# Performance work log

Hardware: AMD Instinct MI355X
Metric: run time of the kernel (lower is better)

Reference implementation:

```python
import jax, jax.numpy as jnp
import numpy as np

B = 512
IN_F = 512
OUT_F = 512
NOISE = 128
OUT_DIM = IN_F * OUT_F + OUT_F  # 262656
PRIOR_SCALE = 1.0


def setup_inputs() -> dict:
    key = jax.random.key(0)
    k_x, k_px, k_n, k_w, k_b, k_pw = jax.random.split(key, 6)
    x = jax.random.normal(k_x, (B, IN_F), dtype=jnp.float32)
    prior_x = jax.random.normal(k_px, (B, IN_F), dtype=jnp.float32)
    hyper_noise = jax.random.normal(k_n, (B, NOISE), dtype=jnp.float32)
    # nn.Linear default init: U(-1/sqrt(fan_in), 1/sqrt(fan_in))
    lim = 1.0 / np.sqrt(NOISE)
    hyper_W = jax.random.uniform(k_w, (OUT_DIM, NOISE), dtype=jnp.float32, minval=-lim, maxval=lim)
    hyper_b = jax.random.uniform(k_b, (OUT_DIM,), dtype=jnp.float32, minval=-lim, maxval=lim)
    # PriorHyperLinear: row-normalized gaussian weight (prior_std=1 -> identity scale), zero bias
    pw = jax.random.normal(k_pw, (OUT_DIM, NOISE), dtype=jnp.float32)
    prior_W = pw / jnp.linalg.norm(pw, axis=1, keepdims=True)
    prior_b = jnp.zeros((OUT_DIM,), dtype=jnp.float32)
    return {"x": x, "prior_x": prior_x, "hyper_noise": hyper_noise,
            "hyper_W": hyper_W, "hyper_b": hyper_b,
            "prior_W": prior_W, "prior_b": prior_b}


def _base_forward(x, params):
    # params: [B, IN_F*OUT_F + OUT_F]
    w = params[:, : IN_F * OUT_F].reshape(-1, IN_F, OUT_F)  # [B, in, out]
    b = params[:, IN_F * OUT_F:]                            # [B, out]
    # bmm([B,1,in],[B,in,out]) + bias -> squeeze -> [B, out]
    return jnp.einsum('bi,bio->bo', x, w) + b


def reference(x, prior_x, hyper_noise, hyper_W, hyper_b, prior_W, prior_b):
    params = hyper_noise @ hyper_W.T + hyper_b            # [B, OUT_DIM]
    out = _base_forward(x, params)
    prior_params = hyper_noise @ prior_W.T + prior_b      # [B, OUT_DIM]
    out = out + _base_forward(prior_x, prior_params) * PRIOR_SCALE
    return out
```

## Files before the change

### kernel.cpp

```cpp
#include <hip/hip_runtime.h>
#include <hip/hip_fp16.h>


#define MAIN_D (512*512)

typedef _Float16 half8 __attribute__((ext_vector_type(8)));
typedef float floatx4 __attribute__((ext_vector_type(4)));

static __device__ __forceinline__ unsigned pk2(float a, float b) {
    union { __half2 h; unsigned u; } c;
    c.h = __float22half2_rn(make_float2(a, b));
    return c.u;
}

__global__ __launch_bounds__(256) void init_kernel(
    const float* __restrict__ hb, const float* __restrict__ pb,
    float* __restrict__ out)
{
    const int idx = blockIdx.x * 256 + threadIdx.x;
    const int o4 = (idx * 4) & 511;
    float4 v;
    v.x = hb[MAIN_D + o4 + 0] + pb[MAIN_D + o4 + 0];
    v.y = hb[MAIN_D + o4 + 1] + pb[MAIN_D + o4 + 1];
    v.z = hb[MAIN_D + o4 + 2] + pb[MAIN_D + o4 + 2];
    v.w = hb[MAIN_D + o4 + 3] + pb[MAIN_D + o4 + 3];
    *(float4*)(out + idx * 4) = v;
}

__global__ __launch_bounds__(512, 2) void main_gemm(
    const float* __restrict__ x, const float* __restrict__ px,
    const float* __restrict__ noise,
    const float* __restrict__ hW, const float* __restrict__ hb,
    const float* __restrict__ pW, const float* __restrict__ pb,
    float* __restrict__ out)
{
    __shared__ __attribute__((aligned(16))) _Float16 Bl[2][128 * 136];
    __shared__ __attribute__((aligned(16))) _Float16 xhl[256 * 40];

    const int t = threadIdx.x;
    const int lin  = blockIdx.x;
    const int s    = (lin >> 3) & 1;
    const int g    = ((lin >> 4) << 3) | (lin & 7);
    const int z    = g >> 2;
    const int y    = g & 3;
    const int b0   = s * 256;
    const int o0   = y * 128;
    const int branch = z >> 4;
    const int ic0  = (z & 15) * 32;
    const float* __restrict__ xsrc = branch ? px : x;
    const float* __restrict__ Ws   = branch ? pW : hW;
    const float* __restrict__ bias = branch ? pb : hb;
    const int nmacro = ((z & 15) == 0) ? 33 : 32;

#pragma unroll
    for (int k = 0; k < 4; ++k) {
        int idx = k * 512 + t;
        int bb = idx >> 3, c = (idx & 7) * 4;
        float4 v = *(const float4*)(xsrc + (b0 + bb) * 512 + ic0 + c);
        *(unsigned*)&xhl[bb * 40 + c]     = pk2(v.x, v.y);
        *(unsigned*)&xhl[bb * 40 + c + 2] = pk2(v.z, v.w);
    }
    _Float16* nzl = &Bl[0][0];
#pragma unroll
    for (int k = 0; k < 16; ++k) {
        int idx = k * 512 + t;
        int bb = idx >> 5, c = (idx & 31) * 4;
        float4 v = *(const float4*)(noise + (b0 + bb) * 128 + c);
        *(unsigned*)&nzl[bb * 136 + c]     = pk2(v.x, v.y);
        *(unsigned*)&nzl[bb * 136 + c + 2] = pk2(v.z, v.w);
    }
    __syncthreads();

    const int lane = t & 63;
    const int w    = t >> 6;
    const int wm64 = (w >> 1) * 64;
    const int wn64 = (w & 1) * 64;
    const int quad = lane >> 4;
    const int l16  = lane & 15;

    half8 nzf[4][4];
#pragma unroll
    for (int mf = 0; mf < 4; ++mf)
#pragma unroll
        for (int q = 0; q < 4; ++q)
            nzf[mf][q] = *(half8*)&nzl[(wm64 + mf * 16 + l16) * 136 + q * 32 + quad * 8];

    floatx4 acc[4][4];
#pragma unroll
    for (int a = 0; a < 4; ++a)
#pragma unroll
        for (int b = 0; b < 4; ++b) acc[a][b] = (floatx4)0.0f;

    float4 wa[4], wb[4];
    {
        const float* p = Ws + (long)(ic0 * 512 + o0) * 128;
#pragma unroll
        for (int j = 0; j < 4; ++j) {
            int c = j * 512 + t;
            int off = (c >> 4) * 128 + (c & 15) * 8;
            wa[j] = *(const float4*)(p + off);
            wb[j] = *(const float4*)(p + off + 4);
        }
    }
    __syncthreads();

    for (int m = 0; m < nmacro; ++m) {
        _Float16* buf = &Bl[m & 1][0];
#pragma unroll
        for (int j = 0; j < 4; ++j) {
            int c = j * 512 + t;
            int row = c >> 4, col8 = (c & 15) * 8;
            *(uint4*)&buf[row * 136 + col8] = make_uint4(
                pk2(wa[j].x, wa[j].y), pk2(wa[j].z, wa[j].w),
                pk2(wb[j].x, wb[j].y), pk2(wb[j].z, wb[j].w));
        }
        __syncthreads();
        if (m + 1 < nmacro) {
            long rb = (m + 1 < 32) ? (long)((ic0 + m + 1) * 512 + o0)
                                   : (long)(MAIN_D + o0);
            const float* p = Ws + rb * 128;
#pragma unroll
            for (int j = 0; j < 4; ++j) {
                int c = j * 512 + t;
                int off = (c >> 4) * 128 + (c & 15) * 8;
                wa[j] = *(const float4*)(p + off);
                wb[j] = *(const float4*)(p + off + 4);
            }
        }
        const bool isE2 = (m >= 32);
        _Float16 xs[4];
        if (!isE2) {
#pragma unroll
            for (int mf = 0; mf < 4; ++mf)
                xs[mf] = xhl[(wm64 + mf * 16 + l16) * 40 + m];
        }
#pragma unroll
        for (int q = 0; q < 4; ++q) {
            half8 bfr[4], afr[4];
#pragma unroll
            for (int nf = 0; nf < 4; ++nf)
                bfr[nf] = *(half8*)&buf[(wn64 + nf * 16 + l16) * 136 + q * 32 + quad * 8];
#pragma unroll
            for (int mf = 0; mf < 4; ++mf) {
                if (isE2) afr[mf] = nzf[mf][q];
                else {
                    half8 xv;
#pragma unroll
                    for (int j = 0; j < 8; ++j) xv[j] = xs[mf];
                    afr[mf] = nzf[mf][q] * xv;
                }
            }
#pragma unroll
            for (int mf = 0; mf < 4; ++mf)
#pragma unroll
                for (int nf = 0; nf < 4; ++nf)
                    acc[mf][nf] = __builtin_amdgcn_mfma_f32_16x16x32_f16(
                        afr[mf], bfr[nf], acc[mf][nf], 0, 0, 0);
        }
    }

    __syncthreads();
    {
        const int oo = t >> 2, kh = (t & 3) * 8;
        float tmp[8];
#pragma unroll
        for (int j = 0; j < 8; ++j)
            tmp[j] = bias[(long)(ic0 + kh + j) * 512 + o0 + oo];
        *(uint4*)&Bl[0][oo * 136 + kh] = make_uint4(
            pk2(tmp[0], tmp[1]), pk2(tmp[2], tmp[3]),
            pk2(tmp[4], tmp[5]), pk2(tmp[6], tmp[7]));
    }
    __syncthreads();
    {
        half8 afr[4], bfr[4];
#pragma unroll
        for (int mf = 0; mf < 4; ++mf)
            afr[mf] = *(half8*)&xhl[(wm64 + mf * 16 + l16) * 40 + quad * 8];
#pragma unroll
        for (int nf = 0; nf < 4; ++nf)
            bfr[nf] = *(half8*)&Bl[0][(wn64 + nf * 16 + l16) * 136 + quad * 8];
#pragma unroll
        for (int mf = 0; mf < 4; ++mf)
#pragma unroll
            for (int nf = 0; nf < 4; ++nf)
                acc[mf][nf] = __builtin_amdgcn_mfma_f32_16x16x32_f16(
                    afr[mf], bfr[nf], acc[mf][nf], 0, 0, 0);
    }

#pragma unroll
    for (int mf = 0; mf < 4; ++mf)
#pragma unroll
        for (int nf = 0; nf < 4; ++nf)
#pragma unroll
            for (int r = 0; r < 4; ++r) {
                int row = b0 + wm64 + mf * 16 + quad * 4 + r;
                int col = o0 + wn64 + nf * 16 + l16;
                atomicAdd(out + row * 512 + col, acc[mf][nf][r]);
            }
}

extern "C" void kernel_launch(void* const* d_in, const int* in_sizes, int n_in,
                              void* d_out, int out_size, void* d_ws, size_t ws_size,
                              hipStream_t stream) {
    const float* x  = (const float*)d_in[0];
    const float* px = (const float*)d_in[1];
    const float* nz = (const float*)d_in[2];
    const float* hW = (const float*)d_in[3];
    const float* hb = (const float*)d_in[4];
    const float* pW = (const float*)d_in[5];
    const float* pb = (const float*)d_in[6];
    float* out = (float*)d_out;

    hipLaunchKernelGGL(init_kernel, dim3(256), dim3(256), 0, stream, hb, pb, out);
    hipLaunchKernelGGL(main_gemm, dim3(256), dim3(512), 0, stream,
                       x, px, nz, hW, hb, pW, pb, out);
}
```

Baseline: 319.9 us.

## Halve output tile width to double grid size and raise occupancy

Shrinks each block's output tile from 128 to 64 columns, doubling the grid to 512 blocks and raising launch bounds to 4 blocks per CU with smaller LDS buffers. Noise fragments are now loaded straight from global memory into registers instead of staging through shared memory, which removes one barrier. MFMA sections are wrapped in s_setprio to favour the matrix issue. The aim is to fill all CUs and hide the memory-bound weight stream. The cost is that noise and x are re-read by twice as many blocks, and there are twice as many atomic adds to the output.

New measurement: 421.5 us. +31.8%, slower.

```diff
diff --git a/kernel.cpp b/kernel.cpp
--- a/kernel.cpp
+++ b/kernel.cpp
@@ -11,6 +11,12 @@
     union { __half2 h; unsigned u; } c;
     c.h = __float22half2_rn(make_float2(a, b));
     return c.u;
+}
+
+static __device__ __forceinline__ half8 mk8(float4 a, float4 b) {
+    union { uint4 u; half8 h; } r;
+    r.u = make_uint4(pk2(a.x, a.y), pk2(a.z, a.w), pk2(b.x, b.y), pk2(b.z, b.w));
+    return r.h;
 }
 
 __global__ __launch_bounds__(256) void init_kernel(
@@ -27,24 +33,24 @@
     *(float4*)(out + idx * 4) = v;
 }
 
-__global__ __launch_bounds__(512, 2) void main_gemm(
+__global__ __launch_bounds__(512, 4) void main_gemm(
     const float* __restrict__ x, const float* __restrict__ px,
     const float* __restrict__ noise,
     const float* __restrict__ hW, const float* __restrict__ hb,
     const float* __restrict__ pW, const float* __restrict__ pb,
     float* __restrict__ out)
 {
-    __shared__ __attribute__((aligned(16))) _Float16 Bl[2][128 * 136];
+    __shared__ __attribute__((aligned(16))) _Float16 Bl[2][64 * 136];
     __shared__ __attribute__((aligned(16))) _Float16 xhl[256 * 40];
 
     const int t = threadIdx.x;
     const int lin  = blockIdx.x;
     const int s    = (lin >> 3) & 1;
     const int g    = ((lin >> 4) << 3) | (lin & 7);
-    const int z    = g >> 2;
-    const int y    = g & 3;
+    const int y    = g & 7;
+    const int z    = g >> 3;
     const int b0   = s * 256;
-    const int o0   = y * 128;
+    const int o0   = y * 64;
     const int branch = z >> 4;
     const int ic0  = (z & 15) * 32;
     const float* __restrict__ xsrc = branch ? px : x;
@@ -52,6 +58,13 @@
     const float* __restrict__ bias = branch ? pb : hb;
     const int nmacro = ((z & 15) == 0) ? 33 : 32;
 
+    const int lane = t & 63;
+    const int w    = t >> 6;
+    const int wm64 = (w >> 1) * 64;
+    const int wn32 = (w & 1) * 32;
+    const int quad = lane >> 4;
+    const int l16  = lane & 15;
+
 #pragma unroll
     for (int k = 0; k < 4; ++k) {
         int idx = k * 512 + t;
@@ -60,54 +73,39 @@
         *(unsigned*)&xhl[bb * 40 + c]     = pk2(v.x, v.y);
         *(unsigned*)&xhl[bb * 40 + c + 2] = pk2(v.z, v.w);
     }
-    _Float16* nzl = &Bl[0][0];
-#pragma unroll
-    for (int k = 0; k < 16; ++k) {
-        int idx = k * 512 + t;
-        int bb = idx >> 5, c = (idx & 31) * 4;
-        float4 v = *(const float4*)(noise + (b0 + bb) * 128 + c);
-        *(unsigned*)&nzl[bb * 136 + c]     = pk2(v.x, v.y);
-        *(unsigned*)&nzl[bb * 136 + c + 2] = pk2(v.z, v.w);
-    }
-    __syncthreads();
-
-    const int lane = t & 63;
-    const int w    = t >> 6;
-    const int wm64 = (w >> 1) * 64;
-    const int wn64 = (w & 1) * 64;
-    const int quad = lane >> 4;
-    const int l16  = lane & 15;
 
     half8 nzf[4][4];
 #pragma unroll
     for (int mf = 0; mf < 4; ++mf)
 #pragma unroll
-        for (int q = 0; q < 4; ++q)
-            nzf[mf][q] = *(half8*)&nzl[(wm64 + mf * 16 + l16) * 136 + q * 32 + quad * 8];
-
-    floatx4 acc[4][4];
+        for (int q = 0; q < 4; ++q) {
+            const float* np = noise + (long)(b0 + wm64 + mf * 16 + l16) * 128
+                            + q * 32 + quad * 8;
+            nzf[mf][q] = mk8(*(const float4*)np, *(const float4*)(np + 4));
+        }
+
+    floatx4 acc[4][2];
 #pragma unroll
     for (int a = 0; a < 4; ++a)
 #pragma unroll
-        for (int b = 0; b < 4; ++b) acc[a][b] = (floatx4)0.0f;
-
-    float4 wa[4], wb[4];
+        for (int b = 0; b < 2; ++b) acc[a][b] = (floatx4)0.0f;
+
+    float4 wa[2], wb[2];
     {
         const float* p = Ws + (long)(ic0 * 512 + o0) * 128;
 #pragma unroll
-        for (int j = 0; j < 4; ++j) {
+        for (int j = 0; j < 2; ++j) {
             int c = j * 512 + t;
             int off = (c >> 4) * 128 + (c & 15) * 8;
             wa[j] = *(const float4*)(p + off);
             wb[j] = *(const float4*)(p + off + 4);
         }
     }
-    __syncthreads();
 
     for (int m = 0; m < nmacro; ++m) {
         _Float16* buf = &Bl[m & 1][0];
 #pragma unroll
-        for (int j = 0; j < 4; ++j) {
+        for (int j = 0; j < 2; ++j) {
             int c = j * 512 + t;
             int row = c >> 4, col8 = (c & 15) * 8;
             *(uint4*)&buf[row * 136 + col8] = make_uint4(
@@ -120,7 +118,7 @@
                                    : (long)(MAIN_D + o0);
             const float* p = Ws + rb * 128;
 #pragma unroll
-            for (int j = 0; j < 4; ++j) {
+            for (int j = 0; j < 2; ++j) {
                 int c = j * 512 + t;
                 int off = (c >> 4) * 128 + (c & 15) * 8;
                 wa[j] = *(const float4*)(p + off);
@@ -136,10 +134,10 @@
         }
 #pragma unroll
         for (int q = 0; q < 4; ++q) {
-            half8 bfr[4], afr[4];
-#pragma unroll
-            for (int nf = 0; nf < 4; ++nf)
-                bfr[nf] = *(half8*)&buf[(wn64 + nf * 16 + l16) * 136 + q * 32 + quad * 8];
+            half8 bfr[2], afr[4];
+#pragma unroll
+            for (int nf = 0; nf < 2; ++nf)
+                bfr[nf] = *(half8*)&buf[(wn32 + nf * 16 + l16) * 136 + q * 32 + quad * 8];
 #pragma unroll
             for (int mf = 0; mf < 4; ++mf) {
                 if (isE2) afr[mf] = nzf[mf][q];
@@ -150,39 +148,40 @@
                     afr[mf] = nzf[mf][q] * xv;
                 }
             }
+            __builtin_amdgcn_s_setprio(1);
 #pragma unroll
             for (int mf = 0; mf < 4; ++mf)
 #pragma unroll
-                for (int nf = 0; nf < 4; ++nf)
+                for (int nf = 0; nf < 2; ++nf)
                     acc[mf][nf] = __builtin_amdgcn_mfma_f32_16x16x32_f16(
                         afr[mf], bfr[nf], acc[mf][nf], 0, 0, 0);
+            __builtin_amdgcn_s_setprio(0);
         }
     }
 
     __syncthreads();
     {
-        const int oo = t >> 2, kh = (t & 3) * 8;
-        float tmp[8];
-#pragma unroll
-        for (int j = 0; j < 8; ++j)
+        const int oo = t >> 3, kh = (t & 7) * 4;
+        float tmp[4];
+#pragma unroll
+        for (int j = 0; j < 4; ++j)
             tmp[j] = bias[(long)(ic0 + kh + j) * 512 + o0 + oo];
-        *(uint4*)&Bl[0][oo * 136 + kh] = make_uint4(
-            pk2(tmp[0], tmp[1]), pk2(tmp[2], tmp[3]),
-            pk2(tmp[4], tmp[5]), pk2(tmp[6], tmp[7]));
+        *(uint2*)&Bl[0][oo * 136 + kh] = make_uint2(
+            pk2(tmp[0], tmp[1]), pk2(tmp[2], tmp[3]));
     }
     __syncthreads();
     {
-        half8 afr[4], bfr[4];
+        half8 afr[4], bfr[2];
 #pragma unroll
         for (int mf = 0; mf < 4; ++mf)
             afr[mf] = *(half8*)&xhl[(wm64 + mf * 16 + l16) * 40 + quad * 8];
 #pragma unroll
-        for (int nf = 0; nf < 4; ++nf)
-            bfr[nf] = *(half8*)&Bl[0][(wn64 + nf * 16 + l16) * 136 + quad * 8];
+        for (int nf = 0; nf < 2; ++nf)
+            bfr[nf] = *(half8*)&Bl[0][(wn32 + nf * 16 + l16) * 136 + quad * 8];
 #pragma unroll
         for (int mf = 0; mf < 4; ++mf)
 #pragma unroll
-            for (int nf = 0; nf < 4; ++nf)
+            for (int nf = 0; nf < 2; ++nf)
                 acc[mf][nf] = __builtin_amdgcn_mfma_f32_16x16x32_f16(
                     afr[mf], bfr[nf], acc[mf][nf], 0, 0, 0);
     }
@@ -190,11 +189,11 @@
 #pragma unroll
     for (int mf = 0; mf < 4; ++mf)
 #pragma unroll
-        for (int nf = 0; nf < 4; ++nf)
+        for (int nf = 0; nf < 2; ++nf)
 #pragma unroll
             for (int r = 0; r < 4; ++r) {
                 int row = b0 + wm64 + mf * 16 + quad * 4 + r;
-                int col = o0 + wn64 + nf * 16 + l16;
+                int col = o0 + wn32 + nf * 16 + l16;
                 atomicAdd(out + row * 512 + col, acc[mf][nf][r]);
             }
 }
@@ -212,6 +211,6 @@
     float* out = (float*)d_out;
 
     hipLaunchKernelGGL(init_kernel, dim3(256), dim3(256), 0, stream, hb, pb, out);
-    hipLaunchKernelGGL(main_gemm, dim3(256), dim3(512), 0, stream,
+    hipLaunchKernelGGL(main_gemm, dim3(512), dim3(512), 0, stream,
                        x, px, nz, hW, hb, pW, pb, out);
 }
```

## Split batch into 128-row tiles, doubling grid, load noise directly to registers

Applied to the files above, without the earlier changes.

The batch tile per block is halved from 256 to 128 rows, and the grid doubles to 512 blocks, so each wave holds a 32x64 accumulator tile instead of 64x64. The noise fragments are now loaded straight from global memory into registers rather than staged through LDS, which removes one barrier. The MFMA sections are wrapped in s_setprio, and launch bounds request 4 blocks per CU. The aim is more occupancy and parallelism, but every weight tile is now streamed by twice as many blocks, which doubles global weight traffic and the number of atomic adds.

Measured after the change: 342.9 us. 1.07x slower.

```diff
diff --git a/kernel.cpp b/kernel.cpp
--- a/kernel.cpp
+++ b/kernel.cpp
@@ -11,6 +11,12 @@
     union { __half2 h; unsigned u; } c;
     c.h = __float22half2_rn(make_float2(a, b));
     return c.u;
+}
+
+static __device__ __forceinline__ half8 mk8(float4 a, float4 b) {
+    union { uint4 u; half8 h; } r;
+    r.u = make_uint4(pk2(a.x, a.y), pk2(a.z, a.w), pk2(b.x, b.y), pk2(b.z, b.w));
+    return r.h;
 }
 
 __global__ __launch_bounds__(256) void init_kernel(
@@ -27,7 +33,7 @@
     *(float4*)(out + idx * 4) = v;
 }
 
-__global__ __launch_bounds__(512, 2) void main_gemm(
+__global__ __launch_bounds__(512, 4) void main_gemm(
     const float* __restrict__ x, const float* __restrict__ px,
     const float* __restrict__ noise,
     const float* __restrict__ hW, const float* __restrict__ hb,
@@ -35,15 +41,15 @@
     float* __restrict__ out)
 {
     __shared__ __attribute__((aligned(16))) _Float16 Bl[2][128 * 136];
-    __shared__ __attribute__((aligned(16))) _Float16 xhl[256 * 40];
+    __shared__ __attribute__((aligned(16))) _Float16 xhl[128 * 40];
 
     const int t = threadIdx.x;
     const int lin  = blockIdx.x;
-    const int s    = (lin >> 3) & 1;
-    const int g    = ((lin >> 4) << 3) | (lin & 7);
+    const int s    = (lin >> 3) & 3;
+    const int g    = ((lin >> 5) << 3) | (lin & 7);
     const int z    = g >> 2;
     const int y    = g & 3;
-    const int b0   = s * 256;
+    const int b0   = s * 128;
     const int o0   = y * 128;
     const int branch = z >> 4;
     const int ic0  = (z & 15) * 32;
@@ -52,42 +58,35 @@
     const float* __restrict__ bias = branch ? pb : hb;
     const int nmacro = ((z & 15) == 0) ? 33 : 32;
 
-#pragma unroll
-    for (int k = 0; k < 4; ++k) {
+    const int lane = t & 63;
+    const int w    = t >> 6;
+    const int wm32 = (w >> 1) * 32;
+    const int wn64 = (w & 1) * 64;
+    const int quad = lane >> 4;
+    const int l16  = lane & 15;
+
+#pragma unroll
+    for (int k = 0; k < 2; ++k) {
         int idx = k * 512 + t;
         int bb = idx >> 3, c = (idx & 7) * 4;
         float4 v = *(const float4*)(xsrc + (b0 + bb) * 512 + ic0 + c);
         *(unsigned*)&xhl[bb * 40 + c]     = pk2(v.x, v.y);
         *(unsigned*)&xhl[bb * 40 + c + 2] = pk2(v.z, v.w);
     }
-    _Float16* nzl = &Bl[0][0];
-#pragma unroll
-    for (int k = 0; k < 16; ++k) {
-        int idx = k * 512 + t;
-        int bb = idx >> 5, c = (idx & 31) * 4;
-        float4 v = *(const float4*)(noise + (b0 + bb) * 128 + c);
-        *(unsigned*)&nzl[bb * 136 + c]     = pk2(v.x, v.y);
-        *(unsigned*)&nzl[bb * 136 + c + 2] = pk2(v.z, v.w);
-    }
-    __syncthreads();
-
-    const int lane = t & 63;
-    const int w    = t >> 6;
-    const int wm64 = (w >> 1) * 64;
-    const int wn64 = (w & 1) * 64;
-    const int quad = lane >> 4;
-    const int l16  = lane & 15;
-
-    half8 nzf[4][4];
-#pragma unroll
-    for (int mf = 0; mf < 4; ++mf)
-#pragma unroll
-        for (int q = 0; q < 4; ++q)
-            nzf[mf][q] = *(half8*)&nzl[(wm64 + mf * 16 + l16) * 136 + q * 32 + quad * 8];
-
-    floatx4 acc[4][4];
-#pragma unroll
-    for (int a = 0; a < 4; ++a)
+
+    half8 nzf[2][4];
+#pragma unroll
+    for (int mf = 0; mf < 2; ++mf)
+#pragma unroll
+        for (int q = 0; q < 4; ++q) {
+            const float* np = noise + (long)(b0 + wm32 + mf * 16 + l16) * 128
+                            + q * 32 + quad * 8;
+            nzf[mf][q] = mk8(*(const float4*)np, *(const float4*)(np + 4));
+        }
+
+    floatx4 acc[2][4];
+#pragma unroll
+    for (int a = 0; a < 2; ++a)
 #pragma unroll
         for (int b = 0; b < 4; ++b) acc[a][b] = (floatx4)0.0f;
 
@@ -102,7 +101,6 @@
             wb[j] = *(const float4*)(p + off + 4);
         }
     }
-    __syncthreads();
 
     for (int m = 0; m < nmacro; ++m) {
         _Float16* buf = &Bl[m & 1][0];
@@ -128,20 +126,20 @@
             }
         }
         const bool isE2 = (m >= 32);
-        _Float16 xs[4];
+        _Float16 xs[2];
         if (!isE2) {
 #pragma unroll
-            for (int mf = 0; mf < 4; ++mf)
-                xs[mf] = xhl[(wm64 + mf * 16 + l16) * 40 + m];
+            for (int mf = 0; mf < 2; ++mf)
+                xs[mf] = xhl[(wm32 + mf * 16 + l16) * 40 + m];
         }
 #pragma unroll
         for (int q = 0; q < 4; ++q) {
-            half8 bfr[4], afr[4];
+            half8 bfr[4], afr[2];
 #pragma unroll
             for (int nf = 0; nf < 4; ++nf)
                 bfr[nf] = *(half8*)&buf[(wn64 + nf * 16 + l16) * 136 + q * 32 + quad * 8];
 #pragma unroll
-            for (int mf = 0; mf < 4; ++mf) {
+            for (int mf = 0; mf < 2; ++mf) {
                 if (isE2) afr[mf] = nzf[mf][q];
                 else {
                     half8 xv;
@@ -150,12 +148,14 @@
                     afr[mf] = nzf[mf][q] * xv;
                 }
             }
-#pragma unroll
-            for (int mf = 0; mf < 4; ++mf)
+            __builtin_amdgcn_s_setprio(1);
+#pragma unroll
+            for (int mf = 0; mf < 2; ++mf)
 #pragma unroll
                 for (int nf = 0; nf < 4; ++nf)
                     acc[mf][nf] = __builtin_amdgcn_mfma_f32_16x16x32_f16(
                         afr[mf], bfr[nf], acc[mf][nf], 0, 0, 0);
+            __builtin_amdgcn_s_setprio(0);
         }
     }
 
@@ -172,15 +172,15 @@
     }
     __syncthreads();
     {
-        half8 afr[4], bfr[4];
-#pragma unroll
-        for (int mf = 0; mf < 4; ++mf)
-            afr[mf] = *(half8*)&xhl[(wm64 + mf * 16 + l16) * 40 + quad * 8];
+        half8 afr[2], bfr[4];
+#pragma unroll
+        for (int mf = 0; mf < 2; ++mf)
+            afr[mf] = *(half8*)&xhl[(wm32 + mf * 16 + l16) * 40 + quad * 8];
 #pragma unroll
         for (int nf = 0; nf < 4; ++nf)
             bfr[nf] = *(half8*)&Bl[0][(wn64 + nf * 16 + l16) * 136 + quad * 8];
 #pragma unroll
-        for (int mf = 0; mf < 4; ++mf)
+        for (int mf = 0; mf < 2; ++mf)
 #pragma unroll
             for (int nf = 0; nf < 4; ++nf)
                 acc[mf][nf] = __builtin_amdgcn_mfma_f32_16x16x32_f16(
@@ -188,12 +188,12 @@
     }
 
 #pragma unroll
-    for (int mf = 0; mf < 4; ++mf)
+    for (int mf = 0; mf < 2; ++mf)
 #pragma unroll
         for (int nf = 0; nf < 4; ++nf)
 #pragma unroll
             for (int r = 0; r < 4; ++r) {
-                int row = b0 + wm64 + mf * 16 + quad * 4 + r;
+                int row = b0 + wm32 + mf * 16 + quad * 4 + r;
                 int col = o0 + wn64 + nf * 16 + l16;
                 atomicAdd(out + row * 512 + col, acc[mf][nf][r]);
             }
@@ -212,6 +212,6 @@
     float* out = (float*)d_out;
 
     hipLaunchKernelGGL(init_kernel, dim3(256), dim3(256), 0, stream, hb, pb, out);
-    hipLaunchKernelGGL(main_gemm, dim3(256), dim3(512), 0, stream,
+    hipLaunchKernelGGL(main_gemm, dim3(512), dim3(512), 0, stream,
                        x, px, nz, hW, hb, pW, pb, out);
 }
```
